# Kernel tuning notes

Hardware: AMD Instinct MI355X
Metric: run time of the kernel (lower is better)

Reference implementation:

```python
import jax, jax.numpy as jnp
import numpy as np

L, D, H = 512, 512, 512  # seq len, input dim, GRU hidden


def setup_inputs() -> dict:
    key = jax.random.key(0)
    ks = jax.random.split(key, 16)
    s = 0.02
    inp = {
        "v": jax.random.normal(ks[0], (L, D), jnp.float32),
        "w1": jax.random.normal(ks[1], (D, D), jnp.float32) * s,
        "b1": jnp.zeros((D,), jnp.float32),
        "w2": jax.random.normal(ks[2], (D, D), jnp.float32) * s,
        "b2": jnp.zeros((D,), jnp.float32),
        # bidirectional GRU, input size 2D, hidden H (PyTorch gate order r,z,n)
        "wih_f": jax.random.normal(ks[3], (3 * H, 2 * D), jnp.float32) * s,
        "whh_f": jax.random.normal(ks[4], (3 * H, H), jnp.float32) * s,
        "bih_f": jnp.zeros((3 * H,), jnp.float32),
        "bhh_f": jnp.zeros((3 * H,), jnp.float32),
        "wih_b": jax.random.normal(ks[5], (3 * H, 2 * D), jnp.float32) * s,
        "whh_b": jax.random.normal(ks[6], (3 * H, H), jnp.float32) * s,
        "bih_b": jnp.zeros((3 * H,), jnp.float32),
        "bhh_b": jnp.zeros((3 * H,), jnp.float32),
    }
    return inp


def _gru_scan(x, wih, whh, bih, bhh, reverse):
    h0 = jnp.zeros((whh.shape[1],), x.dtype)
    gi_all = x @ wih.T + bih  # [L, 3H] precompute input projections

    def step(h, gi):
        gh = h @ whh.T + bhh
        ir, iz, inn = jnp.split(gi, 3)
        hr, hz, hn = jnp.split(gh, 3)
        r = jax.nn.sigmoid(ir + hr)
        z = jax.nn.sigmoid(iz + hz)
        n = jnp.tanh(inn + r * hn)
        hnew = (1.0 - z) * n + z * h
        return hnew, hnew

    _, hs = jax.lax.scan(step, h0, gi_all, reverse=reverse)
    return hs  # [L, H], aligned to original time order


def reference(v, w1, b1, w2, b2, wih_f, whh_f, bih_f, bhh_f, wih_b, whh_b, bih_b, bhh_b):
    # additive self-matching attention: e[t,j] = v_j . tanh(W1 v_j + W2 v_t)
    u = v @ w1.T + b1  # [L, D] (j-side)
    w = v @ w2.T + b2  # [L, D] (t-side)
    t = jnp.tanh(u[None, :, :] + w[:, None, :])  # [L_t, L_j, D]
    e = jnp.einsum("tjd,jd->tj", t, v)  # [L, L]
    a = jax.nn.softmax(e, axis=-1)
    c = a @ v  # [L, D]
    x = jnp.concatenate([v, c], axis=-1)  # [L, 2D]
    hf = _gru_scan(x, wih_f, whh_f, bih_f, bhh_f, reverse=False)
    hb = _gru_scan(x, wih_b, whh_b, bih_b, bhh_b, reverse=True)
    return jnp.concatenate([hf, hb], axis=-1)  # [L, 2H]
```

## Files before the change

kernel.cpp:

```cpp
#include <hip/hip_runtime.h>
#include <hip/hip_bf16.h>


#define L 512
#define DD 512
#define HH 512

__device__ __forceinline__ float tanhf_fast(float x) {
    float ex = __expf(2.f * x);
    return 1.f - __fdividef(2.f, ex + 1.f);
}

__device__ __forceinline__ float sigmoidf_fast(float x) {
    return __fdividef(1.f, 1.f + __expf(-x));
}

template <int BT>
__device__ __forceinline__ void gemm_body(
    const float* __restrict__ A, const float* __restrict__ B,
    const float* __restrict__ bias, float* __restrict__ C,
    int M, int N, int K)
{
    __shared__ float As[16][68];
    __shared__ float Bs[16][68];
    int tid = threadIdx.x;
    int m0 = blockIdx.y * 64, n0 = blockIdx.x * 64;
    int tm = (tid & 15) * 4;
    int tn = (tid >> 4) * 4;
    float acc[4][4] = {};

    for (int k0 = 0; k0 < K; k0 += 16) {
        {
            int c = tid & 15, r0 = tid >> 4;
#pragma unroll
            for (int q = 0; q < 4; q++) {
                int r = r0 + q * 16;
                As[c][r] = A[(size_t)(m0 + r) * K + k0 + c];
            }
        }
        if (BT) {
            int c = tid & 15, r0 = tid >> 4;
#pragma unroll
            for (int q = 0; q < 4; q++) {
                int n = r0 + q * 16;
                Bs[c][n] = B[(size_t)(n0 + n) * K + k0 + c];
            }
        } else {
            int n = tid & 63, r0 = tid >> 6;
#pragma unroll
            for (int q = 0; q < 4; q++) {
                int k = r0 + q * 4;
                Bs[k][n] = B[(size_t)(k0 + k) * N + n0 + n];
            }
        }
        __syncthreads();
#pragma unroll
        for (int k = 0; k < 16; k++) {
            float4 av = *(const float4*)&As[k][tm];
            float4 bv = *(const float4*)&Bs[k][tn];
            float a[4] = {av.x, av.y, av.z, av.w};
            float b[4] = {bv.x, bv.y, bv.z, bv.w};
#pragma unroll
            for (int i = 0; i < 4; i++)
#pragma unroll
                for (int j = 0; j < 4; j++) acc[i][j] += a[i] * b[j];
        }
        __syncthreads();
    }
#pragma unroll
    for (int i = 0; i < 4; i++) {
        float4 o;
        o.x = acc[i][0] + (bias ? bias[n0 + tn + 0] : 0.f);
        o.y = acc[i][1] + (bias ? bias[n0 + tn + 1] : 0.f);
        o.z = acc[i][2] + (bias ? bias[n0 + tn + 2] : 0.f);
        o.w = acc[i][3] + (bias ? bias[n0 + tn + 3] : 0.f);
        *(float4*)&C[(size_t)(m0 + tm + i) * N + n0 + tn] = o;
    }
}

template <int BT>
__global__ __launch_bounds__(256) void gemm_k(
    const float* __restrict__ A, const float* __restrict__ B,
    const float* __restrict__ bias, float* __restrict__ C,
    int M, int N, int K)
{
    gemm_body<BT>(A, B, bias, C, M, N, K);
}

template <int BT>
__global__ __launch_bounds__(256) void gemm2_k(
    const float* __restrict__ A,
    const float* __restrict__ B0, const float* __restrict__ B1,
    const float* __restrict__ bias0, const float* __restrict__ bias1,
    float* __restrict__ C0, float* __restrict__ C1,
    int M, int N, int K)
{
    if (blockIdx.z == 0) gemm_body<BT>(A, B0, bias0, C0, M, N, K);
    else                 gemm_body<BT>(A, B1, bias1, C1, M, N, K);
}

__global__ __launch_bounds__(256) void gemm_gi_k(
    const float* __restrict__ v, const float* __restrict__ cc_,
    const float* __restrict__ B0, const float* __restrict__ B1,
    const float* __restrict__ bias0, const float* __restrict__ bias1,
    float* __restrict__ C0, float* __restrict__ C1)
{
    const float* B    = blockIdx.z ? B1 : B0;
    const float* bias = blockIdx.z ? bias1 : bias0;
    float* C          = blockIdx.z ? C1 : C0;
    const int N = 1536, K = 1024;

    __shared__ float As[16][68];
    __shared__ float Bs[16][68];
    int tid = threadIdx.x;
    int m0 = blockIdx.y * 64, n0 = blockIdx.x * 64;
    int tm = (tid & 15) * 4;
    int tn = (tid >> 4) * 4;
    float acc[4][4] = {};

    for (int k0 = 0; k0 < K; k0 += 16) {
        const float* Asrc = (k0 < 512) ? v : cc_;
        int koff = (k0 < 512) ? k0 : (k0 - 512);
        {
            int c = tid & 15, r0 = tid >> 4;
#pragma unroll
            for (int q = 0; q < 4; q++) {
                int r = r0 + q * 16;
                As[c][r] = Asrc[(size_t)(m0 + r) * 512 + koff + c];
            }
        }
        {
            int c = tid & 15, r0 = tid >> 4;
#pragma unroll
            for (int q = 0; q < 4; q++) {
                int n = r0 + q * 16;
                Bs[c][n] = B[(size_t)(n0 + n) * K + k0 + c];
            }
        }
        __syncthreads();
#pragma unroll
        for (int k = 0; k < 16; k++) {
            float4 av = *(const float4*)&As[k][tm];
            float4 bv = *(const float4*)&Bs[k][tn];
            float a[4] = {av.x, av.y, av.z, av.w};
            float b[4] = {bv.x, bv.y, bv.z, bv.w};
#pragma unroll
            for (int i = 0; i < 4; i++)
#pragma unroll
                for (int j = 0; j < 4; j++) acc[i][j] += a[i] * b[j];
        }
        __syncthreads();
    }
#pragma unroll
    for (int i = 0; i < 4; i++) {
        float4 o;
        o.x = acc[i][0] + bias[n0 + tn + 0];
        o.y = acc[i][1] + bias[n0 + tn + 1];
        o.z = acc[i][2] + bias[n0 + tn + 2];
        o.w = acc[i][3] + bias[n0 + tn + 3];
        *(float4*)&C[(size_t)(m0 + tm + i) * N + n0 + tn] = o;
    }
}

__global__ __launch_bounds__(256) void attn_e_k(
    const float* __restrict__ u, const float* __restrict__ w,
    const float* __restrict__ v, float* __restrict__ e)
{
    __shared__ float wS[16][68];
    __shared__ float uS[32][68];
    __shared__ float vS[32][68];
    int tid = threadIdx.x;
    int t0 = blockIdx.y * 16, j0 = blockIdx.x * 32;
    int tt = tid >> 5, jj = tid & 31;
    float acc0 = 0.f, acc1 = 0.f;

    for (int d0 = 0; d0 < DD; d0 += 64) {
        {
            int c = tid & 63, r0 = tid >> 6;
#pragma unroll
            for (int q = 0; q < 4; q++)
                wS[r0 + q * 4][c] = w[(size_t)(t0 + r0 + q * 4) * DD + d0 + c];
#pragma unroll
            for (int q = 0; q < 8; q++) {
                int r = r0 + q * 4;
                uS[r][c] = u[(size_t)(j0 + r) * DD + d0 + c];
                vS[r][c] = v[(size_t)(j0 + r) * DD + d0 + c];
            }
        }
        __syncthreads();
#pragma unroll
        for (int c4 = 0; c4 < 16; c4++) {
            float4 uv = *(const float4*)&uS[jj][c4 * 4];
            float4 vv = *(const float4*)&vS[jj][c4 * 4];
            float4 w0 = *(const float4*)&wS[tt][c4 * 4];
            float4 w1 = *(const float4*)&wS[tt + 8][c4 * 4];
            acc0 += tanhf_fast(uv.x + w0.x) * vv.x;
            acc0 += tanhf_fast(uv.y + w0.y) * vv.y;
            acc0 += tanhf_fast(uv.z + w0.z) * vv.z;
            acc0 += tanhf_fast(uv.w + w0.w) * vv.w;
            acc1 += tanhf_fast(uv.x + w1.x) * vv.x;
            acc1 += tanhf_fast(uv.y + w1.y) * vv.y;
            acc1 += tanhf_fast(uv.z + w1.z) * vv.z;
            acc1 += tanhf_fast(uv.w + w1.w) * vv.w;
        }
        __syncthreads();
    }
    e[(size_t)(t0 + tt) * L + j0 + jj] = acc0;
    e[(size_t)(t0 + tt + 8) * L + j0 + jj] = acc1;
}

__global__ __launch_bounds__(256) void softmax_k(float* __restrict__ e) {
    int t = blockIdx.x;
    float* row = e + (size_t)t * L;
    int tid = threadIdx.x;
    float v0 = row[tid], v1 = row[tid + 256];
    float m = fmaxf(v0, v1);
#pragma unroll
    for (int off = 32; off > 0; off >>= 1) m = fmaxf(m, __shfl_xor(m, off));
    __shared__ float red[4];
    __shared__ float red2[4];
    int wid = tid >> 6, lane = tid & 63;
    if (lane == 0) red[wid] = m;
    __syncthreads();
    m = fmaxf(fmaxf(red[0], red[1]), fmaxf(red[2], red[3]));
    float e0 = __expf(v0 - m), e1 = __expf(v1 - m);
    float s = e0 + e1;
#pragma unroll
    for (int off = 32; off > 0; off >>= 1) s += __shfl_xor(s, off);
    if (lane == 0) red2[wid] = s;
    __syncthreads();
    s = red2[0] + red2[1] + red2[2] + red2[3];
    float inv = __fdividef(1.f, s);
    row[tid] = e0 * inv;
    row[tid + 256] = e1 * inv;
}

__global__ __launch_bounds__(256) void gru_scan_k(
    const float* __restrict__ whh_f, const float* __restrict__ bhh_f,
    const float* __restrict__ whh_b, const float* __restrict__ bhh_b,
    const float* __restrict__ gi_f, const float* __restrict__ gi_b,
    float* __restrict__ out,
    unsigned* __restrict__ hstage)
{
    int blk = blockIdx.x;
    int dir = blk >> 6;
    int bi = blk & 63;
    int hbase = bi * 8;
    const float* whh = dir ? whh_b : whh_f;
    const float* bhh = dir ? bhh_b : bhh_f;
    const float* gi  = dir ? gi_b : gi_f;
    float* outBase = out + dir * HH;
    unsigned* stage = hstage + dir * 1024;

    __shared__ float hS[HH];
    __shared__ float ghS[24];

    int tid = threadIdx.x;
    int rr = tid >> 3, c8 = tid & 7;
    bool active = rr < 24;

    float4 wreg[16];
    float bhv = 0.f;
    if (active) {
        int g = rr >> 3, i = rr & 7;
        const float4* wrow = (const float4*)(whh + (size_t)(g * HH + hbase + i) * HH);
#pragma unroll
        for (int q = 0; q < 16; q++) wreg[q] = wrow[q * 8 + c8];
        if (c8 == 0) bhv = bhh[g * HH + hbase + i];
    }
    for (int j = tid; j < HH; j += 256) hS[j] = 0.f;

    float ir = 0.f, iz = 0.f, inn = 0.f;
    if (tid < 8) {
        int t0 = dir ? (L - 1) : 0;
        const float* git = gi + (size_t)t0 * (3 * HH);
        ir  = git[hbase + tid];
        iz  = git[HH + hbase + tid];
        inn = git[2 * HH + hbase + tid];
    }
    __syncthreads();

    const float ENC = 4194304.0f;
    const float DEC = 1.0f / 4194304.0f;

    for (int s = 0; s < L; s++) {
        int t = dir ? (L - 1 - s) : s;

        float acc = 0.f;
        if (active) {
            const float4* h4 = (const float4*)hS;
#pragma unroll
            for (int q = 0; q < 16; q++) {
                float4 hv = h4[q * 8 + c8];
                acc += wreg[q].x * hv.x + wreg[q].y * hv.y
                     + wreg[q].z * hv.z + wreg[q].w * hv.w;
            }
            acc += __shfl_xor(acc, 1);
            acc += __shfl_xor(acc, 2);
            acc += __shfl_xor(acc, 4);
            if (c8 == 0) ghS[rr] = acc + bhv;
        }
        __syncthreads();

        if (tid < 8) {
            int i = tid, hg = hbase + i;
            float r = sigmoidf_fast(ir + ghS[i]);
            float z = sigmoidf_fast(iz + ghS[8 + i]);
            float n = tanhf_fast(inn + r * ghS[16 + i]);
            float hnew = (1.f - z) * n + z * hS[hg];
            unsigned enc = ((unsigned)__float2int_rn(hnew * ENC) & 0x00FFFFFFu)
                         | ((unsigned)((s + 1) & 0xFF) << 24);
            __hip_atomic_store(stage + (s & 1) * 512 + hg, enc,
                               __ATOMIC_RELAXED, __HIP_MEMORY_SCOPE_AGENT);
            outBase[(size_t)t * 1024 + hg] = hnew;
        }

        if (s == L - 1) break;

        if (tid < 8) {
            int tn = dir ? (L - 2 - s) : (s + 1);
            const float* git = gi + (size_t)tn * (3 * HH);
            ir  = git[hbase + tid];
            iz  = git[HH + hbase + tid];
            inn = git[2 * HH + hbase + tid];
        }

        {
            unsigned tag = (unsigned)((s + 1) & 0xFF);
            const unsigned long long* src =
                (const unsigned long long*)(stage + (s & 1) * 512) + tid;
            unsigned long long pair;
            unsigned e0, e1;
            do {
                pair = __hip_atomic_load(src, __ATOMIC_RELAXED,
                                         __HIP_MEMORY_SCOPE_AGENT);
                e0 = (unsigned)pair;
                e1 = (unsigned)(pair >> 32);
            } while (((e0 >> 24) != tag) || ((e1 >> 24) != tag));
            float2 hv;
            hv.x = (float)(((int)(e0 << 8)) >> 8) * DEC;
            hv.y = (float)(((int)(e1 << 8)) >> 8) * DEC;
            *(float2*)&hS[2 * tid] = hv;
        }
        __syncthreads();
    }
}

extern "C" void kernel_launch(void* const* d_in, const int* in_sizes, int n_in,
                              void* d_out, int out_size, void* d_ws, size_t ws_size,
                              hipStream_t stream) {
    const float* v     = (const float*)d_in[0];
    const float* w1    = (const float*)d_in[1];
    const float* b1    = (const float*)d_in[2];
    const float* w2    = (const float*)d_in[3];
    const float* b2    = (const float*)d_in[4];
    const float* wih_f = (const float*)d_in[5];
    const float* whh_f = (const float*)d_in[6];
    const float* bih_f = (const float*)d_in[7];
    const float* bhh_f = (const float*)d_in[8];
    const float* wih_b = (const float*)d_in[9];
    const float* whh_b = (const float*)d_in[10];
    const float* bih_b = (const float*)d_in[11];
    const float* bhh_b = (const float*)d_in[12];
    float* out = (float*)d_out;

    float* ws = (float*)d_ws;
    float* u   = ws;
    float* w_  = ws + 262144;
    float* e   = ws + 524288;
    float* c   = ws + 786432;
    float* gif = ws + 1572864;
    float* gib = ws + 2359296;
    unsigned* hstage = (unsigned*)(ws + 3145728);

    gemm2_k<1><<<dim3(8, 8, 2), 256, 0, stream>>>(v, w1, w2, b1, b2, u, w_,
                                                  512, 512, 512);

    attn_e_k<<<dim3(16, 32), 256, 0, stream>>>(u, w_, v, e);
    softmax_k<<<512, 256, 0, stream>>>(e);

    gemm_k<0><<<dim3(8, 8), 256, 0, stream>>>(e, v, nullptr, c, 512, 512, 512);

    gemm_gi_k<<<dim3(24, 8, 2), 256, 0, stream>>>(v, c, wih_f, wih_b,
                                                  bih_f, bih_b, gif, gib);

    gru_scan_k<<<128, 256, 0, stream>>>(whh_f, bhh_f, whh_b, bhh_b,
                                        gif, gib, out, hstage);
}
```

Baseline: 1.328 ms.

## Repartition GRU scan into fewer, larger blocks with wave-level polling

The recurrent GRU kernel now runs 32 blocks of 512 threads, each owning 32 hidden units, instead of 128 blocks of 256 threads owning 8 each. Each wave keeps 12 rows of W_hh in registers, reduces dot products across the full wave, and only wave 0 computes gates and polls the global staging buffer for the other blocks' hidden state. Fewer blocks means fewer participants in the per-step cross-block handoff, and the next-step input gate values are prefetched. The cost is more register pressure, a longer per-block dot product, and serialised polling within a single wave.

New measurement: 2.166 ms. +63.1%, slower.

```diff
diff --git a/kernel.cpp b/kernel.cpp
--- a/kernel.cpp
+++ b/kernel.cpp
@@ -235,7 +235,7 @@
     row[tid + 256] = e1 * inv;
 }
 
-__global__ __launch_bounds__(256) void gru_scan_k(
+__global__ __launch_bounds__(512) void gru_scan_k(
     const float* __restrict__ whh_f, const float* __restrict__ bhh_f,
     const float* __restrict__ whh_b, const float* __restrict__ bhh_b,
     const float* __restrict__ gi_f, const float* __restrict__ gi_b,
@@ -243,9 +243,9 @@
     unsigned* __restrict__ hstage)
 {
     int blk = blockIdx.x;
-    int dir = blk >> 6;
-    int bi = blk & 63;
-    int hbase = bi * 8;
+    int dir = blk >> 4;
+    int bi  = blk & 15;
+    int hbase = bi * 32;
     const float* whh = dir ? whh_b : whh_f;
     const float* bhh = dir ? bhh_b : bhh_f;
     const float* gi  = dir ? gi_b : gi_f;
@@ -253,31 +253,36 @@
     unsigned* stage = hstage + dir * 1024;
 
     __shared__ float hS[HH];
-    __shared__ float ghS[24];
+    __shared__ float ghS[96];
 
     int tid = threadIdx.x;
-    int rr = tid >> 3, c8 = tid & 7;
-    bool active = rr < 24;
-
-    float4 wreg[16];
-    float bhv = 0.f;
-    if (active) {
-        int g = rr >> 3, i = rr & 7;
-        const float4* wrow = (const float4*)(whh + (size_t)(g * HH + hbase + i) * HH);
-#pragma unroll
-        for (int q = 0; q < 16; q++) wreg[q] = wrow[q * 8 + c8];
-        if (c8 == 0) bhv = bhh[g * HH + hbase + i];
-    }
-    for (int j = tid; j < HH; j += 256) hS[j] = 0.f;
-
+    int wv = tid >> 6;
+    int lane = tid & 63;
+
+    float4 wa[12], wb[12];
+#pragma unroll
+    for (int q = 0; q < 12; q++) {
+        int r = wv * 12 + q;
+        int g = r >> 5, i = r & 31;
+        const float* row = whh + (size_t)(g * HH + hbase + i) * HH + lane * 8;
+        wa[q] = *(const float4*)row;
+        wb[q] = *(const float4*)(row + 4);
+    }
+
+    float bhr = 0.f, bhz = 0.f, bhn = 0.f, hp = 0.f;
     float ir = 0.f, iz = 0.f, inn = 0.f;
-    if (tid < 8) {
+    float ir2 = 0.f, iz2 = 0.f, inn2 = 0.f;
+    if (wv == 0 && lane < 32) {
+        bhr = bhh[0 * HH + hbase + lane];
+        bhz = bhh[1 * HH + hbase + lane];
+        bhn = bhh[2 * HH + hbase + lane];
         int t0 = dir ? (L - 1) : 0;
         const float* git = gi + (size_t)t0 * (3 * HH);
-        ir  = git[hbase + tid];
-        iz  = git[HH + hbase + tid];
-        inn = git[2 * HH + hbase + tid];
-    }
+        ir  = git[hbase + lane];
+        iz  = git[HH + hbase + lane];
+        inn = git[2 * HH + hbase + lane];
+    }
+    if (tid < 512) hS[tid] = 0.f;
     __syncthreads();
 
     const float ENC = 4194304.0f;
@@ -286,61 +291,95 @@
     for (int s = 0; s < L; s++) {
         int t = dir ? (L - 1 - s) : s;
 
-        float acc = 0.f;
-        if (active) {
-            const float4* h4 = (const float4*)hS;
-#pragma unroll
-            for (int q = 0; q < 16; q++) {
-                float4 hv = h4[q * 8 + c8];
-                acc += wreg[q].x * hv.x + wreg[q].y * hv.y
-                     + wreg[q].z * hv.z + wreg[q].w * hv.w;
-            }
-            acc += __shfl_xor(acc, 1);
-            acc += __shfl_xor(acc, 2);
-            acc += __shfl_xor(acc, 4);
-            if (c8 == 0) ghS[rr] = acc + bhv;
-        }
-        __syncthreads();
-
-        if (tid < 8) {
-            int i = tid, hg = hbase + i;
-            float r = sigmoidf_fast(ir + ghS[i]);
-            float z = sigmoidf_fast(iz + ghS[8 + i]);
-            float n = tanhf_fast(inn + r * ghS[16 + i]);
-            float hnew = (1.f - z) * n + z * hS[hg];
-            unsigned enc = ((unsigned)__float2int_rn(hnew * ENC) & 0x00FFFFFFu)
-                         | ((unsigned)((s + 1) & 0xFF) << 24);
-            __hip_atomic_store(stage + (s & 1) * 512 + hg, enc,
-                               __ATOMIC_RELAXED, __HIP_MEMORY_SCOPE_AGENT);
-            outBase[(size_t)t * 1024 + hg] = hnew;
-        }
-
-        if (s == L - 1) break;
-
-        if (tid < 8) {
+        if (wv == 0 && lane < 32 && s < L - 1) {
             int tn = dir ? (L - 2 - s) : (s + 1);
             const float* git = gi + (size_t)tn * (3 * HH);
-            ir  = git[hbase + tid];
-            iz  = git[HH + hbase + tid];
-            inn = git[2 * HH + hbase + tid];
-        }
-
-        {
-            unsigned tag = (unsigned)((s + 1) & 0xFF);
-            const unsigned long long* src =
-                (const unsigned long long*)(stage + (s & 1) * 512) + tid;
-            unsigned long long pair;
-            unsigned e0, e1;
-            do {
-                pair = __hip_atomic_load(src, __ATOMIC_RELAXED,
-                                         __HIP_MEMORY_SCOPE_AGENT);
-                e0 = (unsigned)pair;
-                e1 = (unsigned)(pair >> 32);
-            } while (((e0 >> 24) != tag) || ((e1 >> 24) != tag));
-            float2 hv;
-            hv.x = (float)(((int)(e0 << 8)) >> 8) * DEC;
-            hv.y = (float)(((int)(e1 << 8)) >> 8) * DEC;
-            *(float2*)&hS[2 * tid] = hv;
+            ir2  = git[hbase + lane];
+            iz2  = git[HH + hbase + lane];
+            inn2 = git[2 * HH + hbase + lane];
+        }
+
+        float4 h0 = *(const float4*)(hS + lane * 8);
+        float4 h1 = *(const float4*)(hS + lane * 8 + 4);
+        float acc[12];
+#pragma unroll
+        for (int q = 0; q < 12; q++) {
+            acc[q] = wa[q].x * h0.x + wa[q].y * h0.y + wa[q].z * h0.z + wa[q].w * h0.w
+                   + wb[q].x * h1.x + wb[q].y * h1.y + wb[q].z * h1.z + wb[q].w * h1.w;
+        }
+#pragma unroll
+        for (int off = 32; off > 0; off >>= 1) {
+#pragma unroll
+            for (int q = 0; q < 12; q++) acc[q] += __shfl_xor(acc[q], off);
+        }
+        if (lane < 12) ghS[wv * 12 + lane] = acc[lane];
+        __syncthreads();
+
+        if (wv == 0) {
+            if (lane < 32) {
+                float r = sigmoidf_fast(ir + ghS[lane] + bhr);
+                float z = sigmoidf_fast(iz + ghS[32 + lane] + bhz);
+                float n = tanhf_fast(inn + r * (ghS[64 + lane] + bhn));
+                float hnew = (1.f - z) * n + z * hp;
+                hp = hnew;
+                unsigned enc = ((unsigned)__float2int_rn(hnew * ENC) & 0x00FFFFFFu)
+                             | ((unsigned)((s + 1) & 0xFF) << 24);
+                __hip_atomic_store(stage + (s & 1) * 512 + hbase + lane, enc,
+                                   __ATOMIC_RELAXED, __HIP_MEMORY_SCOPE_AGENT);
+                outBase[(size_t)t * 1024 + hbase + lane] = hnew;
+            }
+            ir = ir2; iz = iz2; inn = inn2;
+
+            if (s < L - 1) {
+                unsigned tag = (unsigned)((s + 1) & 0xFF);
+                const unsigned long long* src =
+                    (const unsigned long long*)(stage + (s & 1) * 512);
+                unsigned long long p0 = 0, p1 = 0, p2 = 0, p3 = 0;
+                bool k0 = false, k1 = false, k2 = false, k3 = false;
+                do {
+                    if (!k0) {
+                        p0 = __hip_atomic_load(src + lane, __ATOMIC_RELAXED,
+                                               __HIP_MEMORY_SCOPE_AGENT);
+                        k0 = (((unsigned)(p0 >> 24) & 0xFF) == tag) && ((unsigned)(p0 >> 56) == tag);
+                    }
+                    if (!k1) {
+                        p1 = __hip_atomic_load(src + lane + 64, __ATOMIC_RELAXED,
+                                               __HIP_MEMORY_SCOPE_AGENT);
+                        k1 = (((unsigned)(p1 >> 24) & 0xFF) == tag) && ((unsigned)(p1 >> 56) == tag);
+                    }
+                    if (!k2) {
+                        p2 = __hip_atomic_load(src + lane + 128, __ATOMIC_RELAXED,
+                                               __HIP_MEMORY_SCOPE_AGENT);
+                        k2 = (((unsigned)(p2 >> 24) & 0xFF) == tag) && ((unsigned)(p2 >> 56) == tag);
+                    }
+                    if (!k3) {
+                        p3 = __hip_atomic_load(src + lane + 192, __ATOMIC_RELAXED,
+                                               __HIP_MEMORY_SCOPE_AGENT);
+                        k3 = (((unsigned)(p3 >> 24) & 0xFF) == tag) && ((unsigned)(p3 >> 56) == tag);
+                    }
+                } while (!__all(k0 && k1 && k2 && k3));
+
+                {
+                    unsigned e0, e1;
+                    float2 hv;
+                    e0 = (unsigned)p0; e1 = (unsigned)(p0 >> 32);
+                    hv.x = (float)(((int)(e0 << 8)) >> 8) * DEC;
+                    hv.y = (float)(((int)(e1 << 8)) >> 8) * DEC;
+                    *(float2*)&hS[2 * lane] = hv;
+                    e0 = (unsigned)p1; e1 = (unsigned)(p1 >> 32);
+                    hv.x = (float)(((int)(e0 << 8)) >> 8) * DEC;
+                    hv.y = (float)(((int)(e1 << 8)) >> 8) * DEC;
+                    *(float2*)&hS[2 * (lane + 64)] = hv;
+                    e0 = (unsigned)p2; e1 = (unsigned)(p2 >> 32);
+                    hv.x = (float)(((int)(e0 << 8)) >> 8) * DEC;
+                    hv.y = (float)(((int)(e1 << 8)) >> 8) * DEC;
+                    *(float2*)&hS[2 * (lane + 128)] = hv;
+                    e0 = (unsigned)p3; e1 = (unsigned)(p3 >> 32);
+                    hv.x = (float)(((int)(e0 << 8)) >> 8) * DEC;
+                    hv.y = (float)(((int)(e1 << 8)) >> 8) * DEC;
+                    *(float2*)&hS[2 * (lane + 192)] = hv;
+                }
+            }
         }
         __syncthreads();
     }
@@ -384,6 +423,6 @@
     gemm_gi_k<<<dim3(24, 8, 2), 256, 0, stream>>>(v, c, wih_f, wih_b,
                                                   bih_f, bih_b, gif, gib);
 
-    gru_scan_k<<<128, 256, 0, stream>>>(whh_f, bhh_f, whh_b, bhh_b,
-                                        gif, gib, out, hstage);
-}
+    gru_scan_k<<<32, 512, 0, stream>>>(whh_f, bhh_f, whh_b, bhh_b,
+                                       gif, gib, out, hstage);
+}
```
